# Kernel tuning notes

Hardware: AMD Instinct MI355X
Metric: run time of the kernel (lower is better)

## Reference

```python
import jax, jax.numpy as jnp
import numpy as np

DIM = 768
NUM_HEADS = 12
HEAD_DIM = DIM // NUM_HEADS
HIDDEN = int(DIM * 4.0)
EPS = 1e-8


def layer_norm(x, w, b):
    mu = jnp.mean(x, axis=-1, keepdims=True)
    var = jnp.mean(jnp.square(x - mu), axis=-1, keepdims=True)
    return (x - mu) * jax.lax.rsqrt(var + EPS) * w + b


def setup_inputs() -> dict:
    key = jax.random.key(0)
    ks = jax.random.split(key, 10)
    s = 0.02
    return {
        "x": jax.random.normal(ks[0], (16, 4096, DIM), dtype=jnp.float32),
        # Linear weights stored as [in, out]
        "qkv_w": jax.random.normal(ks[1], (DIM, 3 * DIM), dtype=jnp.float32) * s,
        "qkv_b": jnp.zeros((3 * DIM,), dtype=jnp.float32),
        "proj_w": jax.random.normal(ks[2], (DIM, DIM), dtype=jnp.float32) * s,
        "proj_b": jnp.zeros((DIM,), dtype=jnp.float32),
        "fc1_w": jax.random.normal(ks[3], (DIM, HIDDEN), dtype=jnp.float32) * s,
        "fc1_b": jnp.zeros((HIDDEN,), dtype=jnp.float32),
        "fc2_w": jax.random.normal(ks[4], (HIDDEN, DIM), dtype=jnp.float32) * s,
        "fc2_b": jnp.zeros((DIM,), dtype=jnp.float32),
        "ln1_w": jnp.ones((DIM,), dtype=jnp.float32),
        "ln1_b": jnp.zeros((DIM,), dtype=jnp.float32),
        "ln2_w": jnp.ones((DIM,), dtype=jnp.float32),
        "ln2_b": jnp.zeros((DIM,), dtype=jnp.float32),
    }


def linear_attention(x, qkv_w, qkv_b, proj_w, proj_b):
    B, N, C = x.shape
    qkv = (x @ qkv_w + qkv_b).reshape(B, N, 3, NUM_HEADS, HEAD_DIM)
    qkv = qkv.transpose(2, 0, 3, 1, 4)  # [3, B, H, N, D]
    q, k, v = qkv[0], qkv[1], qkv[2]
    q = jax.nn.elu(q) + 1.0
    k = jax.nn.elu(k) + 1.0
    kv = jnp.einsum('bhsd,bhse->bhde', k, v)          # [B,H,D,D]
    z = 1.0 / jnp.einsum('bhsd,bhd->bhs', q, k.sum(axis=-2))  # [B,H,N]
    out = jnp.einsum('bhde,bhsd,bhs->bhse', kv, q, z)  # [B,H,N,D]
    out = out.transpose(0, 2, 1, 3).reshape(B, N, C)
    return out @ proj_w + proj_b


def reference(x, qkv_w, qkv_b, proj_w, proj_b, fc1_w, fc1_b, fc2_w, fc2_b,
              ln1_w, ln1_b, ln2_w, ln2_b):
    y = linear_attention(layer_norm(x, ln1_w, ln1_b), qkv_w, qkv_b, proj_w, proj_b)
    x = x + y
    h = layer_norm(x, ln2_w, ln2_b)
    h = jax.nn.gelu(h @ fc1_w + fc1_b, approximate=False) @ fc2_w + fc2_b
    return x + h
```

## Files before the change

kernel.cpp:

```cpp
#include <hip/hip_runtime.h>

#define DEVI __device__ __forceinline__

typedef __attribute__((ext_vector_type(8))) short bf16x8;
typedef __attribute__((ext_vector_type(4))) float f32x4;
typedef __attribute__((ext_vector_type(4))) unsigned short usx4;

DEVI float bf2f(unsigned short u) {
  unsigned int b = ((unsigned int)u) << 16;
  float f;
  __builtin_memcpy(&f, &b, 4);
  return f;
}
DEVI unsigned short f2bf(float f) {
  unsigned int x;
  __builtin_memcpy(&x, &f, 4);
  x += 0x7FFFu + ((x >> 16) & 1u);
  return (unsigned short)(x >> 16);
}
DEVI void gload_lds16(const void* g, void* l) {
  __builtin_amdgcn_global_load_lds((const __attribute__((address_space(1))) void*)g,
                                   (__attribute__((address_space(3))) void*)l,
                                   16, 0, 0);
}

__global__ __launch_bounds__(256) void wt_kernel(const float* __restrict__ W,
                                                 unsigned short* __restrict__ Wt,
                                                 int K, int N) {
  __shared__ float t[32][33];
  const int tx = threadIdx.x & 31, ty = threadIdx.x >> 5;
  const int n0 = blockIdx.x * 32, k0 = blockIdx.y * 32;
#pragma unroll
  for (int i = 0; i < 4; ++i)
    t[ty * 4 + i][tx] = W[(size_t)(k0 + ty * 4 + i) * N + n0 + tx];
  __syncthreads();
#pragma unroll
  for (int i = 0; i < 4; ++i)
    Wt[(size_t)(n0 + ty * 4 + i) * K + k0 + tx] = f2bf(t[tx][ty * 4 + i]);
}

__global__ __launch_bounds__(256) void ln_kernel(const float* __restrict__ x,
                                                 const float* __restrict__ w,
                                                 const float* __restrict__ b,
                                                 unsigned short* __restrict__ o) {
  const int lane = threadIdx.x & 63;
  const int wave = threadIdx.x >> 6;
  const size_t row = (size_t)blockIdx.x * 4 + wave;
  const float* xr = x + row * 768;
  float v[12];
  float s = 0.f, sq = 0.f;
#pragma unroll
  for (int i = 0; i < 3; ++i) {
    const float4 f = *(const float4*)&xr[i * 256 + lane * 4];
    v[i * 4 + 0] = f.x; v[i * 4 + 1] = f.y; v[i * 4 + 2] = f.z; v[i * 4 + 3] = f.w;
    s += f.x + f.y + f.z + f.w;
    sq += f.x * f.x + f.y * f.y + f.z * f.z + f.w * f.w;
  }
#pragma unroll
  for (int off = 32; off > 0; off >>= 1) {
    s += __shfl_xor(s, off);
    sq += __shfl_xor(sq, off);
  }
  const float mu = s * (1.f / 768.f);
  const float rs = rsqrtf(sq * (1.f / 768.f) - mu * mu + 1e-8f);
  unsigned short* orow = o + row * 768;
#pragma unroll
  for (int i = 0; i < 3; ++i) {
    usx4 st;
#pragma unroll
    for (int j = 0; j < 4; ++j) {
      const int c = i * 256 + lane * 4 + j;
      st[j] = f2bf((v[i * 4 + j] - mu) * rs * w[c] + b[c]);
    }
    *(usx4*)&orow[i * 256 + lane * 4] = st;
  }
}

__global__ __launch_bounds__(256) void fuse_kernel(const float* __restrict__ x,
                                                   const unsigned short* __restrict__ y,
                                                   const float* __restrict__ w,
                                                   const float* __restrict__ b,
                                                   float* __restrict__ x2,
                                                   unsigned short* __restrict__ o) {
  const int lane = threadIdx.x & 63;
  const int wave = threadIdx.x >> 6;
  const size_t row = (size_t)blockIdx.x * 4 + wave;
  const float* xr = x + row * 768;
  const unsigned short* yr = y + row * 768;
  float* x2r = x2 + row * 768;
  float v[12];
  float s = 0.f, sq = 0.f;
#pragma unroll
  for (int i = 0; i < 3; ++i) {
    const float4 f = *(const float4*)&xr[i * 256 + lane * 4];
    const usx4 yv = *(const usx4*)&yr[i * 256 + lane * 4];
    float t0 = f.x + bf2f(yv[0]);
    float t1 = f.y + bf2f(yv[1]);
    float t2 = f.z + bf2f(yv[2]);
    float t3 = f.w + bf2f(yv[3]);
    v[i * 4 + 0] = t0; v[i * 4 + 1] = t1; v[i * 4 + 2] = t2; v[i * 4 + 3] = t3;
    s += t0 + t1 + t2 + t3;
    sq += t0 * t0 + t1 * t1 + t2 * t2 + t3 * t3;
    float4 fo; fo.x = t0; fo.y = t1; fo.z = t2; fo.w = t3;
    *(float4*)&x2r[i * 256 + lane * 4] = fo;
  }
#pragma unroll
  for (int off = 32; off > 0; off >>= 1) {
    s += __shfl_xor(s, off);
    sq += __shfl_xor(sq, off);
  }
  const float mu = s * (1.f / 768.f);
  const float rs = rsqrtf(sq * (1.f / 768.f) - mu * mu + 1e-8f);
  unsigned short* orow = o + row * 768;
#pragma unroll
  for (int i = 0; i < 3; ++i) {
    usx4 st;
#pragma unroll
    for (int j = 0; j < 4; ++j) {
      const int c = i * 256 + lane * 4 + j;
      st[j] = f2bf((v[i * 4 + j] - mu) * rs * w[c] + b[c]);
    }
    *(usx4*)&orow[i * 256 + lane * 4] = st;
  }
}

template <int EPI>
__global__ __launch_bounds__(512, 2) void gemm256_k(
    const unsigned short* __restrict__ A, const unsigned short* __restrict__ Bt,
    const float* __restrict__ bias, int N, int K,
    unsigned short* __restrict__ O0, unsigned short* __restrict__ O1,
    unsigned short* __restrict__ O2, float* __restrict__ OF) {
  __shared__ char lds[131072];
  const int tid = threadIdx.x;
  const int lane = tid & 63, wave = tid >> 6;
  const int wr = wave >> 2, wc = wave & 3;

  const int gx = gridDim.x;
  const int nwg = gx * gridDim.y;
  const int cpx = nwg >> 3;
  const int wgid = blockIdx.x + gx * blockIdx.y;
  const int v = (wgid & 7) * cpx + (wgid >> 3);
  const size_t n0 = (size_t)(v % gx) * 256;
  const size_t m0 = (size_t)(v / gx) * 256;

  const size_t ldg = (size_t)K * 2;
  const char* Abase = (const char*)A + m0 * ldg;
  const char* Bbase = (const char*)Bt + n0 * ldg;

  const int q0 = tid, q1 = tid + 512;
  const int rp0 = q0 >> 3, rp1 = q1 >> 3;
  const int lc0 = (q0 & 7) ^ (rp0 & 7), lc1 = (q1 & 7) ^ (rp1 & 7);
  const size_t go0 = (size_t)(rp0 * 2 + (lc0 >> 2)) * ldg + (size_t)(lc0 & 3) * 16;
  const size_t go1 = (size_t)(rp1 * 2 + (lc1 >> 2)) * ldg + (size_t)(lc1 & 3) * 16;
  const char* aS0 = Abase + go0;
  const char* aS1 = Abase + go1;
  const char* bS0 = Bbase + go0;
  const char* bS1 = Bbase + go1;
  char* ldsb = (char*)lds;
  const int d0 = tid * 16, d1 = 8192 + tid * 16;

  f32x4 acc[8][4];
#pragma unroll
  for (int m = 0; m < 8; ++m)
#pragma unroll
    for (int n = 0; n < 4; ++n) acc[m][n] = f32x4{0.f, 0.f, 0.f, 0.f};

  const int L = lane & 15;
  const int kc4 = lane >> 4;
  const int pcv = (((L & 1) << 2) | kc4) ^ (L >> 1);
  const int aro = wr * 8192 + (L >> 1) * 128 + pcv * 16;
  const int bro = 16384 + wc * 4096 + (L >> 1) * 128 + pcv * 16;

  const int nt = K >> 5;

#define STAGE_A(tt)                                            \
  do {                                                         \
    char* dst_ = ldsb + ((tt) & 3) * 32768;                    \
    const size_t ko_ = (size_t)(tt) * 64;                      \
    gload_lds16(aS0 + ko_, dst_ + d0);                         \
    gload_lds16(aS1 + ko_, dst_ + d1);                         \
  } while (0)
#define STAGE_B(tt)                                            \
  do {                                                         \
    char* dst_ = ldsb + ((tt) & 3) * 32768;                    \
    const size_t ko_ = (size_t)(tt) * 64;                      \
    gload_lds16(bS0 + ko_, dst_ + 16384 + d0);                 \
    gload_lds16(bS1 + ko_, dst_ + 16384 + d1);                 \
  } while (0)

  STAGE_A(0); STAGE_B(0);
  STAGE_A(1); STAGE_B(1);
  STAGE_A(2); STAGE_B(2);
  asm volatile("s_waitcnt vmcnt(8)" ::: "memory");
  __builtin_amdgcn_s_barrier();

  for (int t = 0; t < nt; ++t) {
    const char* base = ldsb + (t & 3) * 32768;
    bf16x8 bF[4], aF0[4];
#pragma unroll
    for (int n = 0; n < 4; ++n) bF[n] = *(const bf16x8*)(base + bro + n * 1024);
#pragma unroll
    for (int m = 0; m < 4; ++m) aF0[m] = *(const bf16x8*)(base + aro + m * 1024);
    if (t + 3 < nt) STAGE_A(t + 3);
    asm volatile("s_waitcnt lgkmcnt(0)" ::: "memory");
    __builtin_amdgcn_s_barrier();
    __builtin_amdgcn_sched_barrier(0);
    __builtin_amdgcn_s_setprio(1);
#pragma unroll
    for (int m = 0; m < 4; ++m)
#pragma unroll
      for (int n = 0; n < 4; ++n)
        acc[m][n] = __builtin_amdgcn_mfma_f32_16x16x32_bf16(aF0[m], bF[n], acc[m][n], 0, 0, 0);
    __builtin_amdgcn_s_setprio(0);
    __builtin_amdgcn_sched_barrier(0);
    bf16x8 aF1[4];
#pragma unroll
    for (int m = 0; m < 4; ++m) aF1[m] = *(const bf16x8*)(base + aro + (m + 4) * 1024);
    if (t + 3 < nt) STAGE_B(t + 3);
    {
      const int rem = nt - t;
      if (rem >= 4)
        asm volatile("s_waitcnt vmcnt(8) lgkmcnt(0)" ::: "memory");
      else if (rem == 3)
        asm volatile("s_waitcnt vmcnt(4) lgkmcnt(0)" ::: "memory");
      else
        asm volatile("s_waitcnt vmcnt(0) lgkmcnt(0)" ::: "memory");
    }
    __builtin_amdgcn_s_barrier();
    __builtin_amdgcn_sched_barrier(0);
    __builtin_amdgcn_s_setprio(1);
#pragma unroll
    for (int m = 0; m < 4; ++m)
#pragma unroll
      for (int n = 0; n < 4; ++n)
        acc[m + 4][n] = __builtin_amdgcn_mfma_f32_16x16x32_bf16(aF1[m], bF[n], acc[m + 4][n], 0, 0, 0);
    __builtin_amdgcn_s_setprio(0);
    __builtin_amdgcn_sched_barrier(0);
  }
#undef STAGE_A
#undef STAGE_B

  const int rl = (lane >> 4) * 4;
  const int cl = lane & 15;

  if (EPI == 2) {
    const int cbase = (int)n0 + wc * 64;
    const int tsec = cbase / 768;
    const int h = (cbase - tsec * 768) >> 6;
    const int rbase = (int)m0 + wr * 128;
    const int b = rbase >> 12;
    const int s0w = rbase & 4095;
    const size_t bh = (size_t)b * 12 + h;
    if (tsec == 0) {
#pragma unroll
      for (int m = 0; m < 8; ++m)
#pragma unroll
        for (int n = 0; n < 4; ++n) {
          const int d = n * 16 + cl;
          const float bv = bias[cbase + d];
#pragma unroll
          for (int j = 0; j < 4; ++j) {
            float val = acc[m][n][j] + bv;
            val = val > 0.f ? val + 1.f : __expf(val);
            O0[(bh * 4096 + (size_t)(s0w + m * 16 + rl + j)) * 64 + d] = f2bf(val);
          }
        }
    } else {
      unsigned short* dst = (tsec == 1) ? O1 : O2;
      char* wlds = ldsb + wave * 16384;
#pragma unroll
      for (int m = 0; m < 8; ++m)
#pragma unroll
        for (int n = 0; n < 4; ++n) {
          const int c2 = n * 16 + cl;
          const float bv = bias[cbase + c2];
          usx4 st;
#pragma unroll
          for (int j = 0; j < 4; ++j) {
            float val = acc[m][n][j] + bv;
            if (tsec == 1) val = val > 0.f ? val + 1.f : __expf(val);
            st[j] = f2bf(val);
          }
          const int r2 = m * 16 + rl;
          *(usx4*)(wlds + c2 * 256 + ((r2 * 2) ^ ((c2 & 7) << 5))) = st;
        }
      asm volatile("s_waitcnt lgkmcnt(0)" ::: "memory");
#pragma unroll 4
      for (int dl = 0; dl < 64; ++dl) {
        const unsigned int pr =
            *(const unsigned int*)(wlds + dl * 256 + ((lane * 4) ^ ((dl & 7) << 5)));
        *(unsigned int*)&dst[(bh * 64 + dl) * 4096 + (size_t)(s0w + lane * 2)] = pr;
      }
    }
    return;
  }

#pragma unroll
  for (int m = 0; m < 8; ++m) {
    const size_t r0 = m0 + wr * 128 + m * 16 + rl;
#pragma unroll
    for (int n = 0; n < 4; ++n) {
      const size_t c = n0 + wc * 64 + n * 16 + cl;
      const float bv = bias[c];
      if (EPI == 0) {
#pragma unroll
        for (int j = 0; j < 4; ++j) O0[(r0 + j) * (size_t)N + c] = f2bf(acc[m][n][j] + bv);
      } else if (EPI == 1) {
#pragma unroll
        for (int j = 0; j < 4; ++j) {
          float val = acc[m][n][j] + bv;
          val = 0.5f * val * (1.0f + erff(val * 0.70710678118654752f));
          O0[(r0 + j) * (size_t)N + c] = f2bf(val);
        }
      } else {
#pragma unroll
        for (int j = 0; j < 4; ++j) {
          const size_t idx = (r0 + j) * (size_t)N + c;
          OF[idx] += acc[m][n][j] + bv;
        }
      }
    }
  }
}

__global__ __launch_bounds__(256) void kv_kernel(const unsigned short* __restrict__ kT,
                                                 const unsigned short* __restrict__ vT,
                                                 float* __restrict__ kvT) {
  __shared__ float red[4 * 64 * 64];
  const int tid = threadIdx.x;
  const int lane = tid & 63, wave = tid >> 6;
  const size_t bh = blockIdx.x;
  const unsigned short* kb = kT + bh * (size_t)(64 * 4096);
  const unsigned short* vb = vT + bh * (size_t)(64 * 4096);
  f32x4 acc[4][4];
#pragma unroll
  for (int m = 0; m < 4; ++m)
#pragma unroll
    for (int n = 0; n < 4; ++n) acc[m][n] = f32x4{0.f, 0.f, 0.f, 0.f};
  const int kh = (lane >> 4) * 8;
  for (int st = 0; st < 32; ++st) {
    const int s0 = wave * 1024 + st * 32 + kh;
    bf16x8 aF[4], bF[4];
#pragma unroll
    for (int m = 0; m < 4; ++m)
      aF[m] = *(const bf16x8*)&kb[(size_t)((lane & 15) + 16 * m) * 4096 + s0];
#pragma unroll
    for (int n = 0; n < 4; ++n)
      bF[n] = *(const bf16x8*)&vb[(size_t)((lane & 15) + 16 * n) * 4096 + s0];
#pragma unroll
    for (int m = 0; m < 4; ++m)
#pragma unroll
      for (int n = 0; n < 4; ++n)
        acc[m][n] = __builtin_amdgcn_mfma_f32_16x16x32_bf16(aF[m], bF[n], acc[m][n], 0, 0, 0);
  }
#pragma unroll
  for (int m = 0; m < 4; ++m)
#pragma unroll
    for (int n = 0; n < 4; ++n)
#pragma unroll
      for (int j = 0; j < 4; ++j)
        red[wave * 4096 + (m * 16 + (lane >> 4) * 4 + j) * 64 + n * 16 + (lane & 15)] =
            acc[m][n][j];
  __syncthreads();
  for (int i = 0; i < 16; ++i) {
    const int f = i * 256 + tid;
    float s = 0.f;
#pragma unroll
    for (int w = 0; w < 4; ++w) s += red[w * 4096 + f];
    const int d = f >> 6, e = f & 63;
    kvT[bh * 4096 + e * 64 + d] = s;
  }
}

__global__ __launch_bounds__(256) void ksum_kernel(const unsigned short* __restrict__ kT,
                                                   float* __restrict__ ksum) {
  __shared__ float part[256];
  const int tid = threadIdx.x;
  const int d = tid & 63, p = tid >> 6;
  const size_t bh = blockIdx.x;
  const unsigned short* kb = kT + bh * (size_t)(64 * 4096) + (size_t)d * 4096 + p * 1024;
  float s = 0.f;
  for (int i = 0; i < 128; ++i) {
    const bf16x8 v = *(const bf16x8*)&kb[i * 8];
#pragma unroll
    for (int j = 0; j < 8; ++j) s += bf2f((unsigned short)v[j]);
  }
  part[tid] = s;
  __syncthreads();
  if (tid < 64) ksum[bh * 64 + d] = part[d] + part[64 + d] + part[128 + d] + part[192 + d];
}

__global__ __launch_bounds__(256) void attn_out_kernel(const unsigned short* __restrict__ q,
                                                       const float* __restrict__ kvT,
                                                       const float* __restrict__ ksum,
                                                       unsigned short* __restrict__ attnout) {
  __shared__ float kvl[4096];
  __shared__ float ksl[64];
  __shared__ float zl[4 * 64];
  const int tid = threadIdx.x;
  const int lane = tid & 63, wave = tid >> 6;
  const int bh = blockIdx.x >> 2;
  const int chunk = blockIdx.x & 3;
  const int b = bh / 12, h = bh % 12;
  const float* kvb = kvT + (size_t)bh * 4096;
  for (int i = tid; i < 4096; i += 256) kvl[i] = kvb[i];
  if (tid < 64) ksl[tid] = ksum[(size_t)bh * 64 + tid];
  __syncthreads();

  const int kh = (lane >> 4) * 8;
  bf16x8 bF[4], ksF;
#pragma unroll
  for (int n = 0; n < 4; ++n) {
    bf16x8 t;
#pragma unroll
    for (int j = 0; j < 8; ++j)
      t[j] = (short)f2bf(kvl[((lane & 15) + 16 * n) * 64 + kh + j]);
    bF[n] = t;
  }
  {
    bf16x8 t;
#pragma unroll
    for (int j = 0; j < 8; ++j)
      t[j] = ((lane & 15) == 0) ? (short)f2bf(ksl[kh + j]) : (short)0;
    ksF = t;
  }
  const unsigned short* qb = q + (size_t)bh * 4096 * 64;

  for (int st = 0; st < 4; ++st) {
    const int s0 = chunk * 1024 + wave * 256 + st * 64;
    bf16x8 aF[4];
#pragma unroll
    for (int m = 0; m < 4; ++m)
      aF[m] = *(const bf16x8*)&qb[(size_t)(s0 + (lane & 15) + 16 * m) * 64 + kh];
    f32x4 acc[4][4];
    f32x4 dacc[4];
#pragma unroll
    for (int m = 0; m < 4; ++m) {
      dacc[m] = f32x4{0.f, 0.f, 0.f, 0.f};
#pragma unroll
      for (int n = 0; n < 4; ++n) acc[m][n] = f32x4{0.f, 0.f, 0.f, 0.f};
    }
#pragma unroll
    for (int m = 0; m < 4; ++m) {
#pragma unroll
      for (int n = 0; n < 4; ++n)
        acc[m][n] = __builtin_amdgcn_mfma_f32_16x16x32_bf16(aF[m], bF[n], acc[m][n], 0, 0, 0);
      dacc[m] = __builtin_amdgcn_mfma_f32_16x16x32_bf16(aF[m], ksF, dacc[m], 0, 0, 0);
    }
    if ((lane & 15) == 0) {
#pragma unroll
      for (int m = 0; m < 4; ++m)
#pragma unroll
        for (int j = 0; j < 4; ++j)
          zl[wave * 64 + m * 16 + (lane >> 4) * 4 + j] = 1.0f / dacc[m][j];
    }
    __syncthreads();
#pragma unroll
    for (int m = 0; m < 4; ++m)
#pragma unroll
      for (int n = 0; n < 4; ++n)
#pragma unroll
        for (int j = 0; j < 4; ++j) {
          const int sl = m * 16 + (lane >> 4) * 4 + j;
          const int s = s0 + sl;
          const float val = acc[m][n][j] * zl[wave * 64 + sl];
          const int e = n * 16 + (lane & 15);
          attnout[((size_t)b * 4096 + s) * 768 + h * 64 + e] = f2bf(val);
        }
    __syncthreads();
  }
}

extern "C" void kernel_launch(void* const* d_in, const int* in_sizes, int n_in,
                              void* d_out, int out_size, void* d_ws, size_t ws_size,
                              hipStream_t stream) {
  const float* x = (const float*)d_in[0];
  const float* qkv_w = (const float*)d_in[1];
  const float* qkv_b = (const float*)d_in[2];
  const float* proj_w = (const float*)d_in[3];
  const float* proj_b = (const float*)d_in[4];
  const float* fc1_w = (const float*)d_in[5];
  const float* fc1_b = (const float*)d_in[6];
  const float* fc2_w = (const float*)d_in[7];
  const float* fc2_b = (const float*)d_in[8];
  const float* ln1_w = (const float*)d_in[9];
  const float* ln1_b = (const float*)d_in[10];
  const float* ln2_w = (const float*)d_in[11];
  const float* ln2_b = (const float*)d_in[12];
  float* out = (float*)d_out;

  char* ws = (char*)d_ws;
  const size_t PL = (size_t)65536 * 768 * 2;
  unsigned short* xn = (unsigned short*)(ws + 0 * PL);
  unsigned short* q = (unsigned short*)(ws + 1 * PL);
  unsigned short* kT = (unsigned short*)(ws + 2 * PL);
  unsigned short* vT = (unsigned short*)(ws + 3 * PL);
  unsigned short* attnout = xn;
  unsigned short* ybuf = kT;
  unsigned short* xn2 = (unsigned short*)(ws + 4 * PL);
  unsigned short* hbuf = (unsigned short*)(ws + 0 * PL);
  size_t off = 5 * PL;
  float* kvT = (float*)(ws + off); off += (size_t)192 * 4096 * 4;
  float* ksum = (float*)(ws + off); off += (size_t)192 * 64 * 4;
  unsigned short* qkvWt = (unsigned short*)(ws + off); off += (size_t)2304 * 768 * 2;
  unsigned short* projWt = (unsigned short*)(ws + off); off += (size_t)768 * 768 * 2;
  unsigned short* fc1Wt = (unsigned short*)(ws + off); off += (size_t)3072 * 768 * 2;
  unsigned short* fc2Wt = (unsigned short*)(ws + off); off += (size_t)768 * 3072 * 2;

  wt_kernel<<<dim3(72, 24), 256, 0, stream>>>(qkv_w, qkvWt, 768, 2304);
  wt_kernel<<<dim3(24, 24), 256, 0, stream>>>(proj_w, projWt, 768, 768);
  wt_kernel<<<dim3(96, 24), 256, 0, stream>>>(fc1_w, fc1Wt, 768, 3072);
  wt_kernel<<<dim3(24, 96), 256, 0, stream>>>(fc2_w, fc2Wt, 3072, 768);
  ln_kernel<<<16384, 256, 0, stream>>>(x, ln1_w, ln1_b, xn);
  gemm256_k<2><<<dim3(9, 256), 512, 0, stream>>>(xn, qkvWt, qkv_b, 2304, 768, q, kT, vT, nullptr);
  ksum_kernel<<<192, 256, 0, stream>>>(kT, ksum);
  kv_kernel<<<192, 256, 0, stream>>>(kT, vT, kvT);
  attn_out_kernel<<<768, 256, 0, stream>>>(q, kvT, ksum, attnout);
  gemm256_k<0><<<dim3(3, 256), 512, 0, stream>>>(attnout, projWt, proj_b, 768, 768, ybuf, nullptr,
                                                 nullptr, nullptr);
  fuse_kernel<<<16384, 256, 0, stream>>>(x, ybuf, ln2_w, ln2_b, out, xn2);
  gemm256_k<1><<<dim3(12, 256), 512, 0, stream>>>(xn2, fc1Wt, fc1_b, 3072, 768, hbuf, nullptr,
                                                  nullptr, nullptr);
  gemm256_k<3><<<dim3(3, 256), 512, 0, stream>>>(hbuf, fc2Wt, fc2_b, 768, 3072, nullptr, nullptr,
                                                 nullptr, out);
  (void)in_sizes; (void)n_in; (void)out_size; (void)ws_size;
}
```

Before: 1.637 ms.

## Restructure GEMM mainloop to double-buffered BK=64 stages with quarter-step barriers

Replaces the 4-stage BK=32 pipeline, which split A and B loads, with a 2-stage double buffer of BK=64 tiles that loads A and B in a single stage macro. Each iteration now runs four MFMA quarter-blocks separated by barriers, reloading A fragments from LDS per quarter. The goal is fewer loop iterations and simpler waitcnt logic. In exchange the prefetch depth drops to one stage and more barriers are added per iteration, which could expose global-load latency.

```diff
diff --git a/kernel.cpp b/kernel.cpp
--- a/kernel.cpp
+++ b/kernel.cpp
@@ -130,7 +130,7 @@
     const float* __restrict__ bias, int N, int K,
     unsigned short* __restrict__ O0, unsigned short* __restrict__ O1,
     unsigned short* __restrict__ O2, float* __restrict__ OF) {
-  __shared__ char lds[131072];
+  __shared__ unsigned short smem[65536];
   const int tid = threadIdx.x;
   const int lane = tid & 63, wave = tid >> 6;
   const int wr = wave >> 2, wc = wave & 3;
@@ -143,21 +143,16 @@
   const size_t n0 = (size_t)(v % gx) * 256;
   const size_t m0 = (size_t)(v / gx) * 256;
 
-  const size_t ldg = (size_t)K * 2;
-  const char* Abase = (const char*)A + m0 * ldg;
-  const char* Bbase = (const char*)Bt + n0 * ldg;
-
-  const int q0 = tid, q1 = tid + 512;
-  const int rp0 = q0 >> 3, rp1 = q1 >> 3;
-  const int lc0 = (q0 & 7) ^ (rp0 & 7), lc1 = (q1 & 7) ^ (rp1 & 7);
-  const size_t go0 = (size_t)(rp0 * 2 + (lc0 >> 2)) * ldg + (size_t)(lc0 & 3) * 16;
-  const size_t go1 = (size_t)(rp1 * 2 + (lc1 >> 2)) * ldg + (size_t)(lc1 & 3) * 16;
-  const char* aS0 = Abase + go0;
-  const char* aS1 = Abase + go1;
-  const char* bS0 = Bbase + go0;
-  const char* bS1 = Bbase + go1;
-  char* ldsb = (char*)lds;
-  const int d0 = tid * 16, d1 = 8192 + tid * 16;
+  const size_t ldgS = (size_t)K;
+  const unsigned short* Ab = A + m0 * ldgS;
+  const unsigned short* Bb = Bt + n0 * ldgS;
+
+  const int rq0 = tid >> 3;
+  const int c0s = (tid & 7) ^ (rq0 & 7);
+  const size_t sOff0 = (size_t)rq0 * ldgS + (size_t)c0s * 8;
+  const size_t sOff1 = sOff0 + (size_t)64 * ldgS;
+  const unsigned short* srcA1 = Ab + (size_t)128 * ldgS;
+  const unsigned short* srcB1 = Bb + (size_t)128 * ldgS;
 
   f32x4 acc[8][4];
 #pragma unroll
@@ -165,80 +160,89 @@
 #pragma unroll
     for (int n = 0; n < 4; ++n) acc[m][n] = f32x4{0.f, 0.f, 0.f, 0.f};
 
-  const int L = lane & 15;
-  const int kc4 = lane >> 4;
-  const int pcv = (((L & 1) << 2) | kc4) ^ (L >> 1);
-  const int aro = wr * 8192 + (L >> 1) * 128 + pcv * 16;
-  const int bro = 16384 + wc * 4096 + (L >> 1) * 128 + pcv * 16;
-
-  const int nt = K >> 5;
-
-#define STAGE_A(tt)                                            \
-  do {                                                         \
-    char* dst_ = ldsb + ((tt) & 3) * 32768;                    \
-    const size_t ko_ = (size_t)(tt) * 64;                      \
-    gload_lds16(aS0 + ko_, dst_ + d0);                         \
-    gload_lds16(aS1 + ko_, dst_ + d1);                         \
+  const int L = lane & 15, kc4 = lane >> 4;
+  const int sA = wr;
+  const int sB = 2 + (wc >> 1);
+  const int co0 = ((kc4 ^ (L & 7)) << 3);
+  const int co1 = (((4 | kc4) ^ (L & 7)) << 3);
+
+  const int nt2 = K >> 6;
+
+#define STAGE(tt)                                                         \
+  do {                                                                    \
+    unsigned short* sb = &smem[((tt) & 1) * 32768];                       \
+    const size_t ko = (size_t)(tt) * 64;                                  \
+    gload_lds16(Ab + sOff0 + ko, sb + tid * 8);                           \
+    gload_lds16(Ab + sOff1 + ko, sb + 4096 + tid * 8);                    \
+    gload_lds16(srcA1 + sOff0 + ko, sb + 8192 + tid * 8);                 \
+    gload_lds16(srcA1 + sOff1 + ko, sb + 8192 + 4096 + tid * 8);          \
+    gload_lds16(Bb + sOff0 + ko, sb + 16384 + tid * 8);                   \
+    gload_lds16(Bb + sOff1 + ko, sb + 16384 + 4096 + tid * 8);            \
+    gload_lds16(srcB1 + sOff0 + ko, sb + 24576 + tid * 8);                \
+    gload_lds16(srcB1 + sOff1 + ko, sb + 24576 + 4096 + tid * 8);         \
   } while (0)
-#define STAGE_B(tt)                                            \
-  do {                                                         \
-    char* dst_ = ldsb + ((tt) & 3) * 32768;                    \
-    const size_t ko_ = (size_t)(tt) * 64;                      \
-    gload_lds16(bS0 + ko_, dst_ + 16384 + d0);                 \
-    gload_lds16(bS1 + ko_, dst_ + 16384 + d1);                 \
-  } while (0)
-
-  STAGE_A(0); STAGE_B(0);
-  STAGE_A(1); STAGE_B(1);
-  STAGE_A(2); STAGE_B(2);
-  asm volatile("s_waitcnt vmcnt(8)" ::: "memory");
-  __builtin_amdgcn_s_barrier();
-
-  for (int t = 0; t < nt; ++t) {
-    const char* base = ldsb + (t & 3) * 32768;
-    bf16x8 bF[4], aF0[4];
-#pragma unroll
-    for (int n = 0; n < 4; ++n) bF[n] = *(const bf16x8*)(base + bro + n * 1024);
-#pragma unroll
-    for (int m = 0; m < 4; ++m) aF0[m] = *(const bf16x8*)(base + aro + m * 1024);
-    if (t + 3 < nt) STAGE_A(t + 3);
+
+#define MFMA16(AH, BH, MOFF)                                              \
+  __builtin_amdgcn_s_setprio(1);                                          \
+  _Pragma("unroll") for (int m = 0; m < 4; ++m)                           \
+      _Pragma("unroll") for (int n = 0; n < 4; ++n)                       \
+          acc[(MOFF) + m][n] =                                            \
+      __builtin_amdgcn_mfma_f32_16x16x32_bf16(AH[m], BH[n],               \
+                                              acc[(MOFF) + m][n], 0, 0, 0); \
+  __builtin_amdgcn_s_setprio(0);                                          \
+  __builtin_amdgcn_sched_barrier(0)
+
+  STAGE(0);
+
+  for (int t = 0; t < nt2; ++t) {
+    const unsigned short* Arow = &smem[(t & 1) * 32768 + sA * 8192] + L * 64;
+    const unsigned short* Brow =
+        &smem[(t & 1) * 32768 + sB * 8192] + (wc & 1) * 4096 + L * 64;
+    bf16x8 aF[4], bK0[4], bK1[4];
+    if (t + 1 < nt2) {
+      STAGE(t + 1);
+      asm volatile("s_waitcnt vmcnt(8)" ::: "memory");
+    } else {
+      asm volatile("s_waitcnt vmcnt(0)" ::: "memory");
+    }
+    __builtin_amdgcn_s_barrier();
+    asm volatile("" ::: "memory");
+#pragma unroll
+    for (int m = 0; m < 4; ++m) aF[m] = *(const bf16x8*)(Arow + m * 1024 + co0);
+#pragma unroll
+    for (int n = 0; n < 4; ++n) bK0[n] = *(const bf16x8*)(Brow + n * 1024 + co0);
     asm volatile("s_waitcnt lgkmcnt(0)" ::: "memory");
+    __builtin_amdgcn_sched_barrier(0);
+    MFMA16(aF, bK0, 0);
+#pragma unroll
+    for (int m = 0; m < 4; ++m) aF[m] = *(const bf16x8*)(Arow + m * 1024 + co1);
+#pragma unroll
+    for (int n = 0; n < 4; ++n) bK1[n] = *(const bf16x8*)(Brow + n * 1024 + co1);
+    asm volatile("" ::: "memory");
     __builtin_amdgcn_s_barrier();
+    asm volatile("s_waitcnt lgkmcnt(0)" ::: "memory");
     __builtin_amdgcn_sched_barrier(0);
-    __builtin_amdgcn_s_setprio(1);
+    MFMA16(aF, bK1, 0);
 #pragma unroll
     for (int m = 0; m < 4; ++m)
-#pragma unroll
-      for (int n = 0; n < 4; ++n)
-        acc[m][n] = __builtin_amdgcn_mfma_f32_16x16x32_bf16(aF0[m], bF[n], acc[m][n], 0, 0, 0);
-    __builtin_amdgcn_s_setprio(0);
+      aF[m] = *(const bf16x8*)(Arow + 4096 + m * 1024 + co0);
+    asm volatile("" ::: "memory");
+    __builtin_amdgcn_s_barrier();
+    asm volatile("s_waitcnt lgkmcnt(0)" ::: "memory");
     __builtin_amdgcn_sched_barrier(0);
-    bf16x8 aF1[4];
-#pragma unroll
-    for (int m = 0; m < 4; ++m) aF1[m] = *(const bf16x8*)(base + aro + (m + 4) * 1024);
-    if (t + 3 < nt) STAGE_B(t + 3);
-    {
-      const int rem = nt - t;
-      if (rem >= 4)
-        asm volatile("s_waitcnt vmcnt(8) lgkmcnt(0)" ::: "memory");
-      else if (rem == 3)
-        asm volatile("s_waitcnt vmcnt(4) lgkmcnt(0)" ::: "memory");
-      else
-        asm volatile("s_waitcnt vmcnt(0) lgkmcnt(0)" ::: "memory");
-    }
+    MFMA16(aF, bK0, 4);
+#pragma unroll
+    for (int m = 0; m < 4; ++m)
+      aF[m] = *(const bf16x8*)(Arow + 4096 + m * 1024 + co1);
+    asm volatile("" ::: "memory");
     __builtin_amdgcn_s_barrier();
+    asm volatile("s_waitcnt lgkmcnt(0)" ::: "memory");
     __builtin_amdgcn_sched_barrier(0);
-    __builtin_amdgcn_s_setprio(1);
-#pragma unroll
-    for (int m = 0; m < 4; ++m)
-#pragma unroll
-      for (int n = 0; n < 4; ++n)
-        acc[m + 4][n] = __builtin_amdgcn_mfma_f32_16x16x32_bf16(aF1[m], bF[n], acc[m + 4][n], 0, 0, 0);
-    __builtin_amdgcn_s_setprio(0);
-    __builtin_amdgcn_sched_barrier(0);
-  }
-#undef STAGE_A
-#undef STAGE_B
+    MFMA16(aF, bK1, 4);
+    __builtin_amdgcn_s_barrier();
+  }
+#undef STAGE
+#undef MFMA16
 
   const int rl = (lane >> 4) * 4;
   const int cl = lane & 15;
@@ -267,7 +271,7 @@
         }
     } else {
       unsigned short* dst = (tsec == 1) ? O1 : O2;
-      char* wlds = ldsb + wave * 16384;
+      unsigned short* wlds = &smem[wave * 8192];
 #pragma unroll
       for (int m = 0; m < 8; ++m)
 #pragma unroll
@@ -282,13 +286,13 @@
             st[j] = f2bf(val);
           }
           const int r2 = m * 16 + rl;
-          *(usx4*)(wlds + c2 * 256 + ((r2 * 2) ^ ((c2 & 7) << 5))) = st;
+          *(usx4*)&wlds[c2 * 128 + (r2 ^ ((c2 & 7) << 4))] = st;
         }
       asm volatile("s_waitcnt lgkmcnt(0)" ::: "memory");
 #pragma unroll 4
       for (int dl = 0; dl < 64; ++dl) {
         const unsigned int pr =
-            *(const unsigned int*)(wlds + dl * 256 + ((lane * 4) ^ ((dl & 7) << 5)));
+            *(const unsigned int*)&wlds[dl * 128 + ((lane * 2) ^ ((dl & 7) << 4))];
         *(unsigned int*)&dst[(bh * 64 + dl) * 4096 + (size_t)(s0w + lane * 2)] = pr;
       }
     }
```

Result: slower. 1.706 ms (+4.2%).
